# Performance work log

Measured on AMD Instinct MI355X. Metric: run time of the kernel, lower is better.

The kernel has to match this reference:

```python
import jax, jax.numpy as jnp
import numpy as np

CP = (96, 96, 96)      # control-point grid size (D, H, W)
NSTEPS = 7             # VecInt int_steps
N_TP = 4               # timepoints
# all ordered pairs i<j: tid 'ti_to_tj' -> ref=i, flo=j  (K = 6)
REF_IDX = np.array([0, 0, 0, 1, 1, 2])
FLO_IDX = np.array([1, 2, 3, 2, 3, 3])


def _make_grid(shape):
    axes = [jnp.arange(s, dtype=jnp.float32) for s in shape]
    return jnp.stack(jnp.meshgrid(*axes, indexing='ij'), axis=0)  # (3, D, H, W)

GRID = _make_grid(CP)


def trilinear_sample(vol, coords):
    """Sample channels-first volume at absolute voxel coordinates.

    vol:    (C, D, H, W) field values
    coords: (3, D, H, W) absolute (i, j, k) voxel coordinates
    returns (C, D, H, W); border (clamp) handling at edges.
    """
    D, H, W = vol.shape[1:]
    x, y, z = coords[0], coords[1], coords[2]
    x0f = jnp.floor(x); y0f = jnp.floor(y); z0f = jnp.floor(z)
    fx = x - x0f; fy = y - y0f; fz = z - z0f
    x0 = jnp.clip(x0f.astype(jnp.int32), 0, D - 1)
    x1 = jnp.clip(x0 + 1, 0, D - 1)
    y0 = jnp.clip(y0f.astype(jnp.int32), 0, H - 1)
    y1 = jnp.clip(y0 + 1, 0, H - 1)
    z0 = jnp.clip(z0f.astype(jnp.int32), 0, W - 1)
    z1 = jnp.clip(z0 + 1, 0, W - 1)

    c000 = vol[:, x0, y0, z0]; c001 = vol[:, x0, y0, z1]
    c010 = vol[:, x0, y1, z0]; c011 = vol[:, x0, y1, z1]
    c100 = vol[:, x1, y0, z0]; c101 = vol[:, x1, y0, z1]
    c110 = vol[:, x1, y1, z0]; c111 = vol[:, x1, y1, z1]

    c00 = c000 * (1 - fz) + c001 * fz
    c01 = c010 * (1 - fz) + c011 * fz
    c10 = c100 * (1 - fz) + c101 * fz
    c11 = c110 * (1 - fz) + c111 * fz
    c0 = c00 * (1 - fy) + c01 * fy
    c1 = c10 * (1 - fy) + c11 * fy
    return c0 * (1 - fx) + c1 * fx


def vecint(v):
    """Scaling-and-squaring integration of stationary velocity field v: (3,D,H,W)."""
    v = v * (1.0 / 2.0 ** NSTEPS)
    for _ in range(NSTEPS):
        v = v + trilinear_sample(v, GRID + v)
    return v


def compose_fields(f1, f2):
    """(grid + f1 + f2(grid + f1)) - grid, fields (3,D,H,W)."""
    return f1 + trilinear_sample(f2, GRID + f1)


def setup_inputs() -> dict:
    key = jax.random.key(0)
    k1, k2 = jax.random.split(key)
    T = jax.random.normal(k1, (N_TP, 3) + CP, dtype=jnp.float32)
    R = jax.random.normal(k2, CP + (3, len(REF_IDX)), dtype=jnp.float32)
    return {"T": T, "R": R}


def reference(T, R):
    # integrate +/- velocity for every timepoint once (same math as per-pair calls)
    F_pos = jax.vmap(vecint)(T)           # (N, 3, D, H, W) = integrate(T[t])
    F_neg = jax.vmap(vecint)(-T)          # (N, 3, D, H, W) = integrate(-T[t])
    ref = jnp.asarray(REF_IDX)
    flo = jnp.asarray(FLO_IDX)
    # R_hat[k] = compose(integrate(-T[ref_k]), integrate(T[flo_k]))  -> (K,3,D,H,W)
    R_hat = jax.vmap(compose_fields)(F_neg[ref], F_pos[flo])
    # original permutes R_hat to (D,H,W,3,K); equivalently permute R the other way
    residue = R_hat - jnp.transpose(R, (4, 3, 0, 1, 2))  # (K,3,D,H,W)
    # l1 cost: sum_k,x sqrt(sum_c residue^2)
    loss = jnp.sum(jnp.sqrt(jnp.sum(residue ** 2, axis=1)))
    return loss
```

## Files before the change

### kernel.cpp

```cpp
#include <hip/hip_runtime.h>
#include <hip/hip_fp16.h>

#define NV    884736
#define NB    3456
#define DIM   96
#define DIM2  9216


union H4 { uint2 u; __half2 h2[2]; };
union H8 { uint4 u; __half2 h2[4]; };

struct F3 { float x, y, z; };

__device__ __forceinline__ F3 lerp3(F3 a, F3 b, float t, float omt) {
    F3 r;
    r.x = a.x * omt + b.x * t;
    r.y = a.y * omt + b.y * t;
    r.z = a.z * omt + b.z * t;
    return r;
}

__device__ __forceinline__ uint2 pack_h4(float x, float y, float z) {
    H4 v;
    v.h2[0] = __floats2half2_rn(x, y);
    v.h2[1] = __floats2half2_rn(z, 0.0f);
    return v.u;
}

__device__ __forceinline__ F3 unpack_h4(uint2 raw) {
    H4 v; v.u = raw;
    float2 xy = __half22float2(v.h2[0]);
    float2 zp = __half22float2(v.h2[1]);
    F3 r; r.x = xy.x; r.y = xy.y; r.z = zp.x;
    return r;
}

struct TriIdx { int idx[4]; float fx, fy, fz; };

__device__ __forceinline__ TriIdx tri_prep(float x, float y, float z) {
    TriIdx t;
    float xf = floorf(x), yf = floorf(y), zf = floorf(z);
    t.fx = x - xf; t.fy = y - yf;
    float fz = z - zf;
    int x0 = (int)xf; x0 = x0 < 0 ? 0 : (x0 > DIM - 1 ? DIM - 1 : x0);
    int y0 = (int)yf; y0 = y0 < 0 ? 0 : (y0 > DIM - 1 ? DIM - 1 : y0);
    int z0 = (int)zf; z0 = z0 < 0 ? 0 : (z0 > DIM - 1 ? DIM - 1 : z0);
    int x1 = x0 + 1; if (x1 > DIM - 1) x1 = DIM - 1;
    int y1 = y0 + 1; if (y1 > DIM - 1) y1 = DIM - 1;
    t.fz = (z0 < DIM - 1) ? fz : 0.0f;
    int X0 = x0 * DIM2, X1 = x1 * DIM2;
    int Y0 = y0 * DIM,  Y1 = y1 * DIM;
    t.idx[0] = X0 + Y0 + z0;
    t.idx[1] = X0 + Y1 + z0;
    t.idx[2] = X1 + Y0 + z0;
    t.idx[3] = X1 + Y1 + z0;
    return t;
}

__device__ __forceinline__ void tri_gather(const uint2* __restrict__ f,
                                           const TriIdx& t, H8 c[4]) {
    #pragma unroll
    for (int q = 0; q < 4; q++)
        c[q].u = *(const uint4*)(f + t.idx[q]);
}

__device__ __forceinline__ F3 tri_combine(const TriIdx& t, const H8 c[4]) {
    float gz = 1.0f - t.fz, gy = 1.0f - t.fy, gx = 1.0f - t.fx;
    F3 pz[4];
    #pragma unroll
    for (int q = 0; q < 4; q++) {
        float2 xy0 = __half22float2(c[q].h2[0]);
        float2 z0p = __half22float2(c[q].h2[1]);
        float2 xy1 = __half22float2(c[q].h2[2]);
        float2 z1p = __half22float2(c[q].h2[3]);
        F3 lo; lo.x = xy0.x; lo.y = xy0.y; lo.z = z0p.x;
        F3 hi; hi.x = xy1.x; hi.y = xy1.y; hi.z = z1p.x;
        pz[q] = lerp3(lo, hi, t.fz, gz);
    }
    F3 c0 = lerp3(pz[0], pz[1], t.fy, gy);
    F3 c1 = lerp3(pz[2], pz[3], t.fy, gy);
    return lerp3(c0, c1, t.fx, gx);
}

__global__ __launch_bounds__(256) void init_kernel(const float* __restrict__ T,
                                                   uint2* __restrict__ bufA,
                                                   float* __restrict__ out) {
    int t = blockIdx.y;
    int l = blockIdx.x * 256 + threadIdx.x;
    if (t == 0 && l == 0) out[0] = 0.0f;
    const float inv = 1.0f / 128.0f;
    float vx = T[(size_t)(t * 3 + 0) * NV + l] * inv;
    float vy = T[(size_t)(t * 3 + 1) * NV + l] * inv;
    float vz = T[(size_t)(t * 3 + 2) * NV + l] * inv;
    bufA[(size_t)t * NV + l]       = pack_h4( vx,  vy,  vz);
    bufA[(size_t)(t + 4) * NV + l] = pack_h4(-vx, -vy, -vz);
}

__global__ __launch_bounds__(256) void step_kernel(const uint2* __restrict__ src,
                                                   uint2* __restrict__ dst) {
    int g  = blockIdx.x;
    int f  = g & 7;
    int vb = g >> 3;
    const uint2* __restrict__ s = src + (size_t)f * NV;
    uint2*       __restrict__ d = dst + (size_t)f * NV;

    int l   = vb * 256 + threadIdx.x;
    int i   = l / DIM2;
    int rem = l % DIM2;
    int j   = rem / DIM;
    int k   = rem % DIM;

    F3 v = unpack_h4(s[l]);
    TriIdx t = tri_prep((float)i + v.x, (float)j + v.y, (float)k + v.z);
    H8 c[4];
    tri_gather(s, t, c);
    F3 smp = tri_combine(t, c);
    d[l] = pack_h4(v.x + smp.x, v.y + smp.y, v.z + smp.z);
}

__global__ __launch_bounds__(256) void loss_kernel(const uint2* __restrict__ fields,
                                                   const float* __restrict__ R,
                                                   float* __restrict__ out) {
    int l = blockIdx.x * 256 + threadIdx.x;
    int k = l % DIM;
    int j = (l / DIM) % DIM;
    int i = l / DIM2;
    float fi = (float)i, fj = (float)j, fk = (float)k;

    F3 f1c[3];
    #pragma unroll
    for (int r = 0; r < 3; r++)
        f1c[r] = unpack_h4(fields[(size_t)(4 + r) * NV + l]);

    float rbuf[18];
    const float* Rl = R + (size_t)l * 18;
    #pragma unroll
    for (int q = 0; q < 18; q++) rbuf[q] = Rl[q];

    const int REFI[6] = {0, 0, 0, 1, 1, 2};
    const int FLOI[6] = {1, 2, 3, 2, 3, 3};

    float acc = 0.0f;
    #pragma unroll
    for (int p = 0; p < 6; p += 2) {
        F3 f1a = f1c[REFI[p]];
        F3 f1b = f1c[REFI[p + 1]];
        const uint2* __restrict__ f2a = fields + (size_t)FLOI[p]     * NV;
        const uint2* __restrict__ f2b = fields + (size_t)FLOI[p + 1] * NV;
        TriIdx ta = tri_prep(fi + f1a.x, fj + f1a.y, fk + f1a.z);
        TriIdx tb = tri_prep(fi + f1b.x, fj + f1b.y, fk + f1b.z);
        H8 ca[4], cb[4];
        tri_gather(f2a, ta, ca);
        tri_gather(f2b, tb, cb);
        F3 sa = tri_combine(ta, ca);
        F3 sb = tri_combine(tb, cb);
        float rx = f1a.x + sa.x - rbuf[0 * 6 + p];
        float ry = f1a.y + sa.y - rbuf[1 * 6 + p];
        float rz = f1a.z + sa.z - rbuf[2 * 6 + p];
        acc += sqrtf(rx * rx + ry * ry + rz * rz);
        rx = f1b.x + sb.x - rbuf[0 * 6 + p + 1];
        ry = f1b.y + sb.y - rbuf[1 * 6 + p + 1];
        rz = f1b.z + sb.z - rbuf[2 * 6 + p + 1];
        acc += sqrtf(rx * rx + ry * ry + rz * rz);
    }

    __shared__ float wsum[4];
    int lane = threadIdx.x & 63;
    int wid  = threadIdx.x >> 6;
    #pragma unroll
    for (int off = 32; off > 0; off >>= 1)
        acc += __shfl_down(acc, off, 64);
    if (lane == 0) wsum[wid] = acc;
    __syncthreads();
    if (threadIdx.x == 0) {
        float s = wsum[0] + wsum[1] + wsum[2] + wsum[3];
        atomicAdd(out, s);
    }
}

extern "C" void kernel_launch(void* const* d_in, const int* in_sizes, int n_in,
                              void* d_out, int out_size, void* d_ws, size_t ws_size,
                              hipStream_t stream) {
    const float* T = (const float*)d_in[0];
    const float* R = (const float*)d_in[1];
    float* out = (float*)d_out;

    uint2* bufA = (uint2*)d_ws;
    uint2* bufB = bufA + (size_t)8 * NV + 32;

    dim3 blk(256);
    init_kernel<<<dim3(NB, 4), blk, 0, stream>>>(T, bufA, out);

    uint2* src = bufA;
    uint2* dst = bufB;
    for (int s = 0; s < 7; s++) {
        step_kernel<<<NB * 8, blk, 0, stream>>>(src, dst);
        uint2* tmp = src; src = dst; dst = tmp;
    }
    loss_kernel<<<NB, blk, 0, stream>>>(src, R, out);
}
```

Before: 400.1 us.

## Stage field tiles with halo in LDS for scaling-and-squaring steps

Replaces the per-voxel global gather in each integration step with a tiled kernel. Each block loads a cubic tile plus halo of the field into shared memory, and samples from LDS when the displaced point falls inside it, otherwise from global memory. Halo sizes grow for later steps because the displacement grows with each squaring. The aim is to cut redundant global and L2 gather traffic. The cost is extra halo loads, a block barrier, lower occupancy from the large LDS footprint, and divergent fallback paths.

```diff
diff --git a/kernel.cpp b/kernel.cpp
--- a/kernel.cpp
+++ b/kernel.cpp
@@ -35,7 +35,7 @@
     return r;
 }
 
-struct TriIdx { int idx[4]; float fx, fy, fz; };
+struct TriIdx { int x0, y0, z0, x1, y1; float fx, fy, fz; };
 
 __device__ __forceinline__ TriIdx tri_prep(float x, float y, float z) {
     TriIdx t;
@@ -47,21 +47,21 @@
     int z0 = (int)zf; z0 = z0 < 0 ? 0 : (z0 > DIM - 1 ? DIM - 1 : z0);
     int x1 = x0 + 1; if (x1 > DIM - 1) x1 = DIM - 1;
     int y1 = y0 + 1; if (y1 > DIM - 1) y1 = DIM - 1;
+    t.x0 = x0; t.y0 = y0; t.z0 = z0; t.x1 = x1; t.y1 = y1;
     t.fz = (z0 < DIM - 1) ? fz : 0.0f;
-    int X0 = x0 * DIM2, X1 = x1 * DIM2;
-    int Y0 = y0 * DIM,  Y1 = y1 * DIM;
-    t.idx[0] = X0 + Y0 + z0;
-    t.idx[1] = X0 + Y1 + z0;
-    t.idx[2] = X1 + Y0 + z0;
-    t.idx[3] = X1 + Y1 + z0;
     return t;
 }
 
-__device__ __forceinline__ void tri_gather(const uint2* __restrict__ f,
-                                           const TriIdx& t, H8 c[4]) {
-    #pragma unroll
-    for (int q = 0; q < 4; q++)
-        c[q].u = *(const uint4*)(f + t.idx[q]);
+__device__ __forceinline__ void tri_gather_global(const uint2* __restrict__ f,
+                                                  const TriIdx& t, H8 c[4]) {
+    int i00 = t.x0 * DIM2 + t.y0 * DIM + t.z0;
+    int i01 = t.x0 * DIM2 + t.y1 * DIM + t.z0;
+    int i10 = t.x1 * DIM2 + t.y0 * DIM + t.z0;
+    int i11 = t.x1 * DIM2 + t.y1 * DIM + t.z0;
+    c[0].u = *(const uint4*)(f + i00);
+    c[1].u = *(const uint4*)(f + i01);
+    c[2].u = *(const uint4*)(f + i10);
+    c[3].u = *(const uint4*)(f + i11);
 }
 
 __device__ __forceinline__ F3 tri_combine(const TriIdx& t, const H8 c[4]) {
@@ -80,6 +80,10 @@
     F3 c0 = lerp3(pz[0], pz[1], t.fy, gy);
     F3 c1 = lerp3(pz[2], pz[3], t.fy, gy);
     return lerp3(c0, c1, t.fx, gx);
+}
+
+__device__ __forceinline__ int clampi(int v) {
+    return v < 0 ? 0 : (v > DIM - 1 ? DIM - 1 : v);
 }
 
 __global__ __launch_bounds__(256) void init_kernel(const float* __restrict__ T,
@@ -96,26 +100,71 @@
     bufA[(size_t)(t + 4) * NV + l] = pack_h4(-vx, -vy, -vz);
 }
 
-__global__ __launch_bounds__(256) void step_kernel(const uint2* __restrict__ src,
-                                                   uint2* __restrict__ dst) {
-    int g  = blockIdx.x;
-    int f  = g & 7;
-    int vb = g >> 3;
+template<int TS, int HLO, int HHI>
+__global__ __launch_bounds__(256) void step_tile_kernel(const uint2* __restrict__ src,
+                                                        uint2* __restrict__ dst) {
+    constexpr int L  = TS + HLO + HHI;
+    constexpr int L3 = L * L * L;
+    constexpr int NT = DIM / TS;
+    __shared__ uint2 tile[L3];
+
+    int b = blockIdx.x;
+    int f = b & 7;
+    int t = b >> 3;
+    int tz = t % NT;
+    int ty = (t / NT) % NT;
+    int tx = t / (NT * NT);
+    int gx0 = tx * TS, gy0 = ty * TS, gz0 = tz * TS;
+    int ox = gx0 - HLO, oy = gy0 - HLO, oz = gz0 - HLO;
+
     const uint2* __restrict__ s = src + (size_t)f * NV;
     uint2*       __restrict__ d = dst + (size_t)f * NV;
 
-    int l   = vb * 256 + threadIdx.x;
-    int i   = l / DIM2;
-    int rem = l % DIM2;
-    int j   = rem / DIM;
-    int k   = rem % DIM;
-
-    F3 v = unpack_h4(s[l]);
-    TriIdx t = tri_prep((float)i + v.x, (float)j + v.y, (float)k + v.z);
-    H8 c[4];
-    tri_gather(s, t, c);
-    F3 smp = tri_combine(t, c);
-    d[l] = pack_h4(v.x + smp.x, v.y + smp.y, v.z + smp.z);
+    for (int n = threadIdx.x; n < L3; n += 256) {
+        int lz = n % L;
+        int ly = (n / L) % L;
+        int lx = n / (L * L);
+        int gx = clampi(ox + lx), gy = clampi(oy + ly), gz = clampi(oz + lz);
+        tile[n] = s[gx * DIM2 + gy * DIM + gz];
+    }
+    __syncthreads();
+
+    for (int n = threadIdx.x; n < TS * TS * TS; n += 256) {
+        int lz = n % TS;
+        int ly = (n / TS) % TS;
+        int lx = n / (TS * TS);
+        int gi = gx0 + lx, gj = gy0 + ly, gk = gz0 + lz;
+
+        F3 v = unpack_h4(tile[(lx + HLO) * (L * L) + (ly + HLO) * L + (lz + HLO)]);
+        TriIdx tr = tri_prep((float)gi + v.x, (float)gj + v.y, (float)gk + v.z);
+
+        int lx0 = tr.x0 - ox, lx1 = tr.x1 - ox;
+        int ly0 = tr.y0 - oy, ly1 = tr.y1 - oy;
+        int lz0 = tr.z0 - oz;
+        bool inb = (lx0 >= 0) & (lx1 <= L - 1) &
+                   (ly0 >= 0) & (ly1 <= L - 1) &
+                   (lz0 >= 0) & (lz0 <= L - 2);
+
+        H8 c[4];
+        if (inb) {
+            int b00 = lx0 * (L * L) + ly0 * L + lz0;
+            int b01 = lx0 * (L * L) + ly1 * L + lz0;
+            int b10 = lx1 * (L * L) + ly0 * L + lz0;
+            int b11 = lx1 * (L * L) + ly1 * L + lz0;
+            uint2 a0 = tile[b00], a1 = tile[b00 + 1];
+            uint2 b0 = tile[b01], b1 = tile[b01 + 1];
+            uint2 c0 = tile[b10], c1 = tile[b10 + 1];
+            uint2 d0 = tile[b11], d1 = tile[b11 + 1];
+            c[0].u = make_uint4(a0.x, a0.y, a1.x, a1.y);
+            c[1].u = make_uint4(b0.x, b0.y, b1.x, b1.y);
+            c[2].u = make_uint4(c0.x, c0.y, c1.x, c1.y);
+            c[3].u = make_uint4(d0.x, d0.y, d1.x, d1.y);
+        } else {
+            tri_gather_global(s, tr, c);
+        }
+        F3 smp = tri_combine(tr, c);
+        d[gi * DIM2 + gj * DIM + gk] = pack_h4(v.x + smp.x, v.y + smp.y, v.z + smp.z);
+    }
 }
 
 __global__ __launch_bounds__(256) void loss_kernel(const uint2* __restrict__ fields,
@@ -150,8 +199,8 @@
         TriIdx ta = tri_prep(fi + f1a.x, fj + f1a.y, fk + f1a.z);
         TriIdx tb = tri_prep(fi + f1b.x, fj + f1b.y, fk + f1b.z);
         H8 ca[4], cb[4];
-        tri_gather(f2a, ta, ca);
-        tri_gather(f2b, tb, cb);
+        tri_gather_global(f2a, ta, ca);
+        tri_gather_global(f2b, tb, cb);
         F3 sa = tri_combine(ta, ca);
         F3 sb = tri_combine(tb, cb);
         float rx = f1a.x + sa.x - rbuf[0 * 6 + p];
@@ -193,9 +242,14 @@
 
     uint2* src = bufA;
     uint2* dst = bufB;
-    for (int s = 0; s < 7; s++) {
-        step_kernel<<<NB * 8, blk, 0, stream>>>(src, dst);
+    for (int s = 0; s < 5; s++) {
+        step_tile_kernel<16, 1, 2><<<6 * 6 * 6 * 8, blk, 0, stream>>>(src, dst);
         uint2* tmp = src; src = dst; dst = tmp;
     }
+    step_tile_kernel<12, 2, 3><<<8 * 8 * 8 * 8, blk, 0, stream>>>(src, dst);
+    { uint2* tmp = src; src = dst; dst = tmp; }
+    step_tile_kernel<12, 3, 4><<<8 * 8 * 8 * 8, blk, 0, stream>>>(src, dst);
+    { uint2* tmp = src; src = dst; dst = tmp; }
+
     loss_kernel<<<NB, blk, 0, stream>>>(src, R, out);
 }
```

Result: slower. 620.2 us (+55.0%).
